# Kernel tuning notes

Hardware: AMD Instinct MI355X
Metric: run time of the kernel (lower is better)

The kernel has to match this reference:

```python
import jax, jax.numpy as jnp
import numpy as np

IN_DIM, HID_DIM, CNV1_DIM, BATCH = 4096, 2048, 1024, 16384


def setup_inputs() -> dict:
    key = jax.random.key(0)
    ks = jax.random.split(key, 12)
    x = jax.random.normal(ks[0], (BATCH, IN_DIM), dtype=jnp.float32)
    mask_ih = jax.random.randint(ks[1], (HID_DIM, IN_DIM), 0, 2).astype(jnp.bool_)
    mask_hc = jax.random.randint(ks[2], (CNV1_DIM, HID_DIM), 0, 2).astype(jnp.bool_)
    # SparseLinear params (Linear-style: weight [out,in], bias [out])
    lim_ih = 1.0 / np.sqrt(IN_DIM)
    w_ih = jax.random.uniform(ks[3], (HID_DIM, IN_DIM), jnp.float32, -lim_ih, lim_ih)
    b_ih = jax.random.uniform(ks[4], (HID_DIM,), jnp.float32, -lim_ih, lim_ih)
    lim_hc = 1.0 / np.sqrt(HID_DIM)
    w_hc = jax.random.uniform(ks[5], (CNV1_DIM, HID_DIM), jnp.float32, -lim_hc, lim_hc)
    b_hc = jax.random.uniform(ks[6], (CNV1_DIM,), jnp.float32, -lim_hc, lim_hc)
    # Conv1d(1,1,2) weights, kaiming_uniform(tanh): gain=5/3, fan_in=2
    bound = (5.0 / 3.0) * np.sqrt(3.0 / 2.0)
    w_c1 = jax.random.uniform(ks[7], (2,), jnp.float32, -bound, bound)
    w_c2 = jax.random.uniform(ks[8], (2,), jnp.float32, -bound, bound)
    lim_c = 1.0 / np.sqrt(2.0)
    b_c1 = jax.random.uniform(ks[9], (), jnp.float32, -lim_c, lim_c)
    b_c2 = jax.random.uniform(ks[10], (), jnp.float32, -lim_c, lim_c)
    return {"x": x, "mask_ih": mask_ih, "mask_hc": mask_hc,
            "w_ih": w_ih, "b_ih": b_ih, "w_hc": w_hc, "b_hc": b_hc,
            "w_c1": w_c1, "b_c1": b_c1, "w_c2": w_c2, "b_c2": b_c2}


def _conv1d_k2s2(x, w, b):
    # Conv1d(1,1,kernel=2,stride=2) on [B, L] == pairwise reshape + dot
    B, L = x.shape
    return jnp.einsum('blk,k->bl', x.reshape(B, L // 2, 2), w) + b


def reference(x, mask_ih, mask_hc, w_ih, b_ih, w_hc, b_hc, w_c1, b_c1, w_c2, b_c2):
    h = jnp.tanh(x @ (w_ih * mask_ih).T + b_ih)            # [B, HID]
    c = jnp.tanh(h @ (w_hc * mask_hc).T + b_hc)            # [B, CNV1]
    y = jnp.tanh(_conv1d_k2s2(c, w_c1, b_c1))              # [B, CNV1/2]
    y = jnp.tanh(_conv1d_k2s2(y, w_c2, b_c2))              # [B, CNV1/4]
    return y
```

## Files before the change

### kernel.cpp

```cpp
#include <hip/hip_runtime.h>
#include <cstdint>
#include <cstddef>

typedef __bf16  bf16x8f __attribute__((ext_vector_type(8)));
typedef unsigned short u16x8 __attribute__((ext_vector_type(8)));
typedef float   f32x16 __attribute__((ext_vector_type(16)));

__device__ __forceinline__ unsigned short f2bf(float f) {
    union { float f; uint32_t u; } c; c.f = f;
    uint32_t u = c.u;
    return (unsigned short)((u + 0x7fffu + ((u >> 16) & 1u)) >> 16);
}

__device__ __forceinline__ float fast_tanh(float x) {
    float e = __builtin_exp2f(2.885390081777927f * x);
    return 1.0f - 2.0f * __builtin_amdgcn_rcpf(e + 1.0f);
}

__device__ __forceinline__ void load16_lds(const void* g, unsigned short* l) {
    __builtin_amdgcn_global_load_lds(
        (const __attribute__((address_space(1))) unsigned int*)g,
        (__attribute__((address_space(3))) unsigned int*)l,
        16, 0, 0);
}

__global__ __launch_bounds__(256)
void detect_mask(const unsigned char* __restrict__ m, int* __restrict__ flag) {
    __shared__ int s_gt1, s_off;
    if (threadIdx.x == 0) { s_gt1 = 0; s_off = 0; }
    __syncthreads();
    int gt1 = 0, off = 0;
    for (int k = threadIdx.x; k < 4096; k += 256) {
        unsigned char b = m[k];
        if (b > 1) gt1 = 1;
        if ((k & 3) && b) off = 1;
    }
    if (gt1) atomicOr(&s_gt1, 1);
    if (off) atomicOr(&s_off, 1);
    __syncthreads();
    if (threadIdx.x == 0) *flag = (!s_gt1 && s_off) ? 1 : 0;
}

__global__ __launch_bounds__(256)
void cast_f32_bf16(const float* __restrict__ in, unsigned short* __restrict__ out, int n) {
    int tid = blockIdx.x * blockDim.x + threadIdx.x;
    int stride = gridDim.x * blockDim.x;
    for (int e = tid * 4; e < n; e += stride * 4) {
        float4 v = *(const float4*)(in + e);
        ushort4 o;
        o.x = f2bf(v.x); o.y = f2bf(v.y); o.z = f2bf(v.z); o.w = f2bf(v.w);
        *(ushort4*)(out + e) = o;
    }
}

__global__ __launch_bounds__(256)
void mask_cast(const float* __restrict__ w, const void* __restrict__ mv,
               const int* __restrict__ flag, unsigned short* __restrict__ out, int n) {
    const bool u8 = (*flag != 0);
    int tid = blockIdx.x * blockDim.x + threadIdx.x;
    int stride = gridDim.x * blockDim.x;
    for (int e = tid * 4; e < n; e += stride * 4) {
        float4 v = *(const float4*)(w + e);
        int m0, m1, m2, m3;
        if (u8) {
            uchar4 mm = *(const uchar4*)((const unsigned char*)mv + e);
            m0 = mm.x; m1 = mm.y; m2 = mm.z; m3 = mm.w;
        } else {
            int4 mm = ((const int4*)mv)[e >> 2];
            m0 = mm.x; m1 = mm.y; m2 = mm.z; m3 = mm.w;
        }
        ushort4 o;
        o.x = m0 ? f2bf(v.x) : (unsigned short)0;
        o.y = m1 ? f2bf(v.y) : (unsigned short)0;
        o.z = m2 ? f2bf(v.z) : (unsigned short)0;
        o.w = m3 ? f2bf(v.w) : (unsigned short)0;
        *(ushort4*)(out + e) = o;
    }
}

template <typename OutT, bool FUSE>
__global__ __launch_bounds__(256)
void gemm32(const unsigned short* __restrict__ A,
            const unsigned short* __restrict__ W,
            const float* __restrict__ bias,
            OutT* __restrict__ out,
            const float* __restrict__ w1, const float* __restrict__ b1,
            const float* __restrict__ w2, const float* __restrict__ b2,
            int M, int N, int K, int lbx) {
    __shared__ unsigned short As[128 * 32];
    __shared__ unsigned short Bs[128 * 32];

    const int t    = threadIdx.x;
    const int lane = t & 63;
    const int wave = t >> 6;
    const int wrow = (wave >> 1) * 64;
    const int wcol = (wave & 1) * 64;
    const int l31  = lane & 31;
    const int lh   = lane >> 5;
    const int swz  = (l31 >> 1) & 3;

    const int id = blockIdx.x;
    const int bx = (id >> 3) & ((1 << lbx) - 1);
    const int by = (id & 7) | ((id >> (3 + lbx)) << 3);
    const int bm = by * 128;
    const int bn = bx * 128;

    const int c0 = t, c1 = t + 256;
    const int row0 = c0 >> 2, row1 = c1 >> 2;
    const int cc0 = (c0 & 3) ^ ((row0 >> 1) & 3);
    const int cc1 = (c1 & 3) ^ ((row1 >> 1) & 3);
    const uint32_t va0 = (uint32_t)(row0 * K + cc0 * 8) * 2;
    const uint32_t va1 = (uint32_t)(row1 * K + cc1 * 8) * 2;
    const char* Au = (const char*)(A + (size_t)bm * K);
    const char* Wu = (const char*)(W + (size_t)bn * K);

    f32x16 acc[2][2] = {};

    for (int k0 = 0; k0 < K; k0 += 32) {
        const char* Ak = Au + (size_t)(k0 * 2);
        const char* Wk = Wu + (size_t)(k0 * 2);
        load16_lds(Ak + va0, As + c0 * 8);
        load16_lds(Ak + va1, As + c1 * 8);
        load16_lds(Wk + va0, Bs + c0 * 8);
        load16_lds(Wk + va1, Bs + c1 * 8);
        __syncthreads();

        u16x8 a[2][2], b[2][2];
#pragma unroll
        for (int s = 0; s < 2; ++s) {
            int q = (s * 2 + lh) ^ swz;
#pragma unroll
            for (int i = 0; i < 2; ++i) {
                a[i][s] = ((const u16x8*)As)[(wrow + i * 32 + l31) * 4 + q];
                b[i][s] = ((const u16x8*)Bs)[(wcol + i * 32 + l31) * 4 + q];
            }
        }
#pragma unroll
        for (int s = 0; s < 2; ++s)
#pragma unroll
            for (int i = 0; i < 2; ++i)
#pragma unroll
                for (int j = 0; j < 2; ++j)
                    acc[i][j] = __builtin_amdgcn_mfma_f32_32x32x16_bf16(
                        __builtin_bit_cast(bf16x8f, a[i][s]),
                        __builtin_bit_cast(bf16x8f, b[j][s]),
                        acc[i][j], 0, 0, 0);
        __syncthreads();
    }

    float w10 = 0, w11 = 0, bb1 = 0, w20 = 0, w21 = 0, bb2 = 0;
    if constexpr (FUSE) {
        w10 = w1[0]; w11 = w1[1]; bb1 = b1[0];
        w20 = w2[0]; w21 = w2[1]; bb2 = b2[0];
    }
#pragma unroll
    for (int j = 0; j < 2; ++j) {
        const int gn = bn + wcol + j * 32 + l31;
        const float bv = bias[gn];
#pragma unroll
        for (int i = 0; i < 2; ++i) {
#pragma unroll
            for (int reg = 0; reg < 16; ++reg) {
                const int gm = bm + wrow + i * 32 + (reg & 3) + 8 * (reg >> 2) + 4 * lh;
                float c = fast_tanh(acc[i][j][reg] + bv);
                if constexpr (FUSE) {
                    float c1 = __shfl_xor(c, 1);
                    float c2 = __shfl_xor(c, 2);
                    float c3 = __shfl_xor(c, 3);
                    float y10 = fast_tanh(w10 * c  + w11 * c1 + bb1);
                    float y11 = fast_tanh(w10 * c2 + w11 * c3 + bb1);
                    float y   = fast_tanh(w20 * y10 + w21 * y11 + bb2);
                    if ((lane & 3) == 0)
                        out[(size_t)gm * (N >> 2) + (gn >> 2)] = (OutT)y;
                } else {
                    out[(size_t)gm * N + gn] = (OutT)f2bf(c);
                }
            }
        }
    }
}

extern "C" void kernel_launch(void* const* d_in, const int* in_sizes, int n_in,
                              void* d_out, int out_size, void* d_ws, size_t ws_size,
                              hipStream_t stream) {
    constexpr int B   = 16384;
    constexpr int IN  = 4096;
    constexpr int HID = 2048;
    constexpr int CNV = 1024;

    const float* x       = (const float*)d_in[0];
    const void*  mask_ih = d_in[1];
    const void*  mask_hc = d_in[2];
    const float* w_ih    = (const float*)d_in[3];
    const float* b_ih    = (const float*)d_in[4];
    const float* w_hc    = (const float*)d_in[5];
    const float* b_hc    = (const float*)d_in[6];
    const float* w_c1    = (const float*)d_in[7];
    const float* b_c1    = (const float*)d_in[8];
    const float* w_c2    = (const float*)d_in[9];
    const float* b_c2    = (const float*)d_in[10];
    float* out = (float*)d_out;

    char* ws = (char*)d_ws;
    unsigned short* Xb  = (unsigned short*)(ws);
    unsigned short* Wih = (unsigned short*)(ws + 134217728);
    unsigned short* Whc = (unsigned short*)(ws + 150994944);
    unsigned short* Hb  = (unsigned short*)(ws + 155189248);
    int*            flag = (int*)(ws + 222298112);

    detect_mask<<<1, 256, 0, stream>>>((const unsigned char*)mask_ih, flag);

    cast_f32_bf16<<<4096, 256, 0, stream>>>(x, Xb, B * IN);
    mask_cast<<<1024, 256, 0, stream>>>(w_ih, mask_ih, flag, Wih, HID * IN);
    mask_cast<<<256, 256, 0, stream>>>(w_hc, mask_hc, flag, Whc, CNV * HID);

    gemm32<unsigned short, false><<<2048, 256, 0, stream>>>(
        Xb, Wih, b_ih, Hb, nullptr, nullptr, nullptr, nullptr, B, HID, IN, 4);

    gemm32<float, true><<<1024, 256, 0, stream>>>(
        Hb, Whc, b_hc, out, w_c1, b_c1, w_c2, b_c2, B, CNV, HID, 3);
}
```

Baseline: 906.7 us.

## Replace GEMM with 256x256 tiled, double-buffered LDS pipelined MFMA kernel

Replaces the 128x128 single-buffered GEMM with a 512-thread 256x256 tile kernel that prefetches A and B slices into double-buffered LDS using direct global-to-LDS loads, interleaved with MFMA phases under fine-grained barriers and vmcnt waits. This aims to raise arithmetic intensity per block and hide global memory latency behind matrix math. It uses 128KB of LDS per block, which limits occupancy. The second GEMM now launches only 256 blocks, risking underfilled CUs.

```diff
diff --git a/kernel.cpp b/kernel.cpp
--- a/kernel.cpp
+++ b/kernel.cpp
@@ -79,74 +79,127 @@
 }
 
 template <typename OutT, bool FUSE>
-__global__ __launch_bounds__(256)
-void gemm32(const unsigned short* __restrict__ A,
-            const unsigned short* __restrict__ W,
-            const float* __restrict__ bias,
-            OutT* __restrict__ out,
-            const float* __restrict__ w1, const float* __restrict__ b1,
-            const float* __restrict__ w2, const float* __restrict__ b2,
-            int M, int N, int K, int lbx) {
-    __shared__ unsigned short As[128 * 32];
-    __shared__ unsigned short Bs[128 * 32];
+__global__ __launch_bounds__(512, 2)
+void gemm256(const unsigned short* __restrict__ A,
+             const unsigned short* __restrict__ W,
+             const float* __restrict__ bias,
+             OutT* __restrict__ out,
+             const float* __restrict__ w1, const float* __restrict__ b1,
+             const float* __restrict__ w2, const float* __restrict__ b2,
+             int N, int K, int lbx) {
+    __shared__ __align__(16) unsigned short lds[65536];
 
     const int t    = threadIdx.x;
     const int lane = t & 63;
     const int wave = t >> 6;
-    const int wrow = (wave >> 1) * 64;
-    const int wcol = (wave & 1) * 64;
     const int l31  = lane & 31;
     const int lh   = lane >> 5;
-    const int swz  = (l31 >> 1) & 3;
+    const int wrow = (wave >> 2) * 128;
+    const int wcol = (wave & 3) * 64;
 
     const int id = blockIdx.x;
-    const int bx = (id >> 3) & ((1 << lbx) - 1);
-    const int by = (id & 7) | ((id >> (3 + lbx)) << 3);
-    const int bm = by * 128;
-    const int bn = bx * 128;
-
-    const int c0 = t, c1 = t + 256;
-    const int row0 = c0 >> 2, row1 = c1 >> 2;
-    const int cc0 = (c0 & 3) ^ ((row0 >> 1) & 3);
-    const int cc1 = (c1 & 3) ^ ((row1 >> 1) & 3);
-    const uint32_t va0 = (uint32_t)(row0 * K + cc0 * 8) * 2;
-    const uint32_t va1 = (uint32_t)(row1 * K + cc1 * 8) * 2;
+    const int bx = id & ((1 << lbx) - 1);
+    const int by = id >> lbx;
+    const int bm = by * 256, bn = bx * 256;
+
     const char* Au = (const char*)(A + (size_t)bm * K);
     const char* Wu = (const char*)(W + (size_t)bn * K);
 
-    f32x16 acc[2][2] = {};
-
-    for (int k0 = 0; k0 < K; k0 += 32) {
-        const char* Ak = Au + (size_t)(k0 * 2);
-        const char* Wk = Wu + (size_t)(k0 * 2);
-        load16_lds(Ak + va0, As + c0 * 8);
-        load16_lds(Ak + va1, As + c1 * 8);
-        load16_lds(Wk + va0, Bs + c0 * 8);
-        load16_lds(Wk + va1, Bs + c1 * 8);
-        __syncthreads();
-
-        u16x8 a[2][2], b[2][2];
-#pragma unroll
-        for (int s = 0; s < 2; ++s) {
-            int q = (s * 2 + lh) ^ swz;
-#pragma unroll
-            for (int i = 0; i < 2; ++i) {
-                a[i][s] = ((const u16x8*)As)[(wrow + i * 32 + l31) * 4 + q];
-                b[i][s] = ((const u16x8*)Bs)[(wcol + i * 32 + l31) * 4 + q];
-            }
-        }
-#pragma unroll
-        for (int s = 0; s < 2; ++s)
-#pragma unroll
-            for (int i = 0; i < 2; ++i)
-#pragma unroll
-                for (int j = 0; j < 2; ++j)
-                    acc[i][j] = __builtin_amdgcn_mfma_f32_32x32x16_bf16(
-                        __builtin_bit_cast(bf16x8f, a[i][s]),
-                        __builtin_bit_cast(bf16x8f, b[j][s]),
-                        acc[i][j], 0, 0, 0);
-        __syncthreads();
-    }
+    uint32_t aSrc[2], bSrc[2][2];
+#pragma unroll
+    for (int j = 0; j < 2; ++j) {
+        const int u = t + j * 512;
+        { const int r = u >> 2, c = u & 3;
+          aSrc[j] = (uint32_t)((r * K + ((c ^ (r & 3)) << 3)) * 2); }
+        { const int rl = u >> 3, c = u & 7;
+#pragma unroll
+          for (int Un = 0; Un < 2; ++Un) {
+              const int n = (rl & 31) + ((rl >> 5) << 6) + Un * 32;
+              bSrc[Un][j] = (uint32_t)((n * K + ((c ^ (n & 7)) << 3)) * 2);
+          } }
+    }
+
+    int aRow[4];
+#pragma unroll
+    for (int mt = 0; mt < 4; ++mt) aRow[mt] = (wrow + mt * 32 + l31) * 32;
+    int aSwz[2];
+#pragma unroll
+    for (int j = 0; j < 2; ++j) aSwz[j] = ((j * 2 + lh) ^ (l31 & 3)) << 3;
+    int bBase[2];
+#pragma unroll
+    for (int nt = 0; nt < 2; ++nt)
+        bBase[nt] = 16384 + ((((wcol >> 5) + nt) & 1) * 8192)
+                  + (((wcol + nt * 32) >> 6) * 2048) + l31 * 64;
+    int bSwz[4];
+#pragma unroll
+    for (int kp = 0; kp < 2; ++kp)
+#pragma unroll
+        for (int j = 0; j < 2; ++j)
+            bSwz[kp * 2 + j] = ((kp * 4 + j * 2 + lh) ^ (l31 & 7)) << 3;
+
+#define STAGE_A(buf, Uk, kB) do {                                              \
+    const char* g_ = Au + (kB);                                                \
+    unsigned short* l_ = lds + (buf) * 32768 + (Uk) * 8192 + t * 8;            \
+    load16_lds(g_ + aSrc[0] + (Uk) * 64, l_);                                  \
+    load16_lds(g_ + aSrc[1] + (Uk) * 64, l_ + 4096);                           \
+} while (0)
+
+#define STAGE_B(buf, Un, kB) do {                                              \
+    const char* g_ = Wu + (kB);                                                \
+    unsigned short* l_ = lds + (buf) * 32768 + 16384 + (Un) * 8192 + t * 8;    \
+    load16_lds(g_ + bSrc[Un][0], l_);                                          \
+    load16_lds(g_ + bSrc[Un][1], l_ + 4096);                                   \
+} while (0)
+
+#define BAR    asm volatile("s_barrier" ::: "memory")
+#define VM4BAR do { asm volatile("s_waitcnt vmcnt(4)" ::: "memory"); BAR; } while (0)
+
+#define PHASE(buf, nt, kp, STAGE_STMT) do {                                    \
+    u16x8 aF[4][2], bF[2];                                                     \
+    const unsigned short* Lb_ = lds + (buf) * 32768;                           \
+    _Pragma("unroll")                                                          \
+    for (int j_ = 0; j_ < 2; ++j_) {                                           \
+        _Pragma("unroll")                                                      \
+        for (int mt_ = 0; mt_ < 4; ++mt_)                                      \
+            aF[mt_][j_] = *(const u16x8*)(Lb_ + (kp) * 8192 + aRow[mt_] + aSwz[j_]); \
+        bF[j_] = *(const u16x8*)(Lb_ + bBase[nt] + bSwz[(kp) * 2 + j_]);       \
+    }                                                                          \
+    STAGE_STMT;                                                                \
+    BAR;                                                                       \
+    __builtin_amdgcn_s_setprio(1);                                             \
+    _Pragma("unroll")                                                          \
+    for (int j_ = 0; j_ < 2; ++j_)                                             \
+        _Pragma("unroll")                                                      \
+        for (int mt_ = 0; mt_ < 4; ++mt_)                                      \
+            acc[mt_][nt] = __builtin_amdgcn_mfma_f32_32x32x16_bf16(            \
+                __builtin_bit_cast(bf16x8f, aF[mt_][j_]),                      \
+                __builtin_bit_cast(bf16x8f, bF[j_]), acc[mt_][nt], 0, 0, 0);   \
+    __builtin_amdgcn_s_setprio(0);                                             \
+} while (0)
+
+    f32x16 acc[4][2] = {};
+
+    STAGE_A(0, 0, 0); STAGE_A(0, 1, 0); STAGE_B(0, 0, 0); STAGE_B(0, 1, 0);
+    STAGE_A(1, 0, 128); STAGE_B(1, 0, 128);
+    asm volatile("s_waitcnt vmcnt(4)" ::: "memory");
+    BAR;
+
+    const int KB = K * 2;
+    const int KL = KB - 128;
+    for (int k0 = 0; k0 < KB; k0 += 256) {
+        const int kA = k0 + 128;
+        int kB1 = k0 + 256; if (kB1 > KL) kB1 = KL;
+        int kB2 = k0 + 384; if (kB2 > KL) kB2 = KL;
+        PHASE(0, 0, 0, STAGE_A(1, 1, kA));  BAR;
+        PHASE(0, 1, 0, STAGE_B(1, 1, kA));  BAR;
+        PHASE(0, 0, 1, STAGE_A(0, 0, kB1)); BAR;
+        PHASE(0, 1, 1, STAGE_B(0, 0, kB1)); VM4BAR;
+        PHASE(1, 0, 0, STAGE_A(0, 1, kB1)); BAR;
+        PHASE(1, 1, 0, STAGE_B(0, 1, kB1)); BAR;
+        PHASE(1, 0, 1, STAGE_A(1, 0, kB2)); BAR;
+        PHASE(1, 1, 1, STAGE_B(1, 0, kB2)); VM4BAR;
+    }
+    asm volatile("s_waitcnt vmcnt(0)" ::: "memory");
 
     float w10 = 0, w11 = 0, bb1 = 0, w20 = 0, w21 = 0, bb2 = 0;
     if constexpr (FUSE) {
@@ -154,15 +207,15 @@
         w20 = w2[0]; w21 = w2[1]; bb2 = b2[0];
     }
 #pragma unroll
-    for (int j = 0; j < 2; ++j) {
-        const int gn = bn + wcol + j * 32 + l31;
+    for (int nt = 0; nt < 2; ++nt) {
+        const int gn = bn + wcol + nt * 32 + l31;
         const float bv = bias[gn];
 #pragma unroll
-        for (int i = 0; i < 2; ++i) {
+        for (int mt = 0; mt < 4; ++mt) {
 #pragma unroll
             for (int reg = 0; reg < 16; ++reg) {
-                const int gm = bm + wrow + i * 32 + (reg & 3) + 8 * (reg >> 2) + 4 * lh;
-                float c = fast_tanh(acc[i][j][reg] + bv);
+                const int gm = bm + wrow + mt * 32 + (reg & 3) + 8 * (reg >> 2) + 4 * lh;
+                float c = fast_tanh(acc[mt][nt][reg] + bv);
                 if constexpr (FUSE) {
                     float c1 = __shfl_xor(c, 1);
                     float c2 = __shfl_xor(c, 2);
@@ -178,6 +231,11 @@
             }
         }
     }
+#undef STAGE_A
+#undef STAGE_B
+#undef BAR
+#undef VM4BAR
+#undef PHASE
 }
 
 extern "C" void kernel_launch(void* const* d_in, const int* in_sizes, int n_in,
@@ -214,9 +272,9 @@
     mask_cast<<<1024, 256, 0, stream>>>(w_ih, mask_ih, flag, Wih, HID * IN);
     mask_cast<<<256, 256, 0, stream>>>(w_hc, mask_hc, flag, Whc, CNV * HID);
 
-    gemm32<unsigned short, false><<<2048, 256, 0, stream>>>(
-        Xb, Wih, b_ih, Hb, nullptr, nullptr, nullptr, nullptr, B, HID, IN, 4);
-
-    gemm32<float, true><<<1024, 256, 0, stream>>>(
-        Hb, Whc, b_hc, out, w_c1, b_c1, w_c2, b_c2, B, CNV, HID, 3);
-}
+    gemm256<unsigned short, false><<<512, 512, 0, stream>>>(
+        Xb, Wih, b_ih, Hb, nullptr, nullptr, nullptr, nullptr, HID, IN, 3);
+
+    gemm256<float, true><<<256, 512, 0, stream>>>(
+        Hb, Whc, b_hc, out, w_c1, b_c1, w_c2, b_c2, CNV, HID, 2);
+}
```

Result: slower. 940.6 us (+3.7%).
